# Kernel tuning notes

Hardware: AMD Instinct MI355X
Metric: run time of the kernel (lower is better)

## Reference

```python
import jax, jax.numpy as jnp
import numpy as np

NUM_HEADS = 12
THETA = 10000.0


def _rope(x, pos):
    # x: [B, H, S, dk]; interleaved even/odd pair rotation
    dk = x.shape[-1]
    freqs = THETA ** (-jnp.arange(dk // 2, dtype=jnp.float32) * 2.0 / dk)  # [dk/2]
    ang = pos.astype(jnp.float32)[:, None] * freqs                         # [S, dk/2]
    cos, sin = jnp.cos(ang), jnp.sin(ang)
    x1, x2 = x[..., 0::2], x[..., 1::2]
    rot = jnp.stack([x1 * cos - x2 * sin, x1 * sin + x2 * cos], axis=-1)
    return rot.reshape(x.shape)


def setup_inputs() -> dict:
    key = jax.random.key(0)
    ks = jax.random.split(key, 5)
    B, S, D = 4, 2048, 768
    w_scale = 1.0 / np.sqrt(D).astype(np.float32)
    x = jax.random.normal(ks[0], (B, S, D), dtype=jnp.float32)
    Wq = jax.random.normal(ks[1], (D, D), dtype=jnp.float32) * w_scale
    Wk = jax.random.normal(ks[2], (D, D), dtype=jnp.float32) * w_scale
    Wv = jax.random.normal(ks[3], (D, D), dtype=jnp.float32) * w_scale
    Wo = jax.random.normal(ks[4], (D, D), dtype=jnp.float32) * w_scale
    token_positions = jnp.arange(S, dtype=jnp.int32)
    return {"x": x, "Wq": Wq, "Wk": Wk, "Wv": Wv, "Wo": Wo,
            "token_positions": token_positions}


def reference(x, Wq, Wk, Wv, Wo, token_positions):
    B, S, D = x.shape
    H = NUM_HEADS
    dk = D // H
    # bias-free linear layers: y = x @ W^T (torch Linear weight convention)
    q = (x @ Wq.T).reshape(B, S, H, dk).transpose(0, 2, 1, 3)  # [B,H,S,dk]
    k = (x @ Wk.T).reshape(B, S, H, dk).transpose(0, 2, 1, 3)
    v = (x @ Wv.T).reshape(B, S, H, dk).transpose(0, 2, 1, 3)
    q = _rope(q, token_positions)
    k = _rope(k, token_positions)
    scores = jnp.einsum('bhqd,bhkd->bhqk', q, k) / np.float32(np.sqrt(dk))
    causal = jnp.tril(jnp.ones((S, S), dtype=bool))
    scores = jnp.where(causal, scores, -jnp.inf)
    attn = jax.nn.softmax(scores, axis=-1)                      # [B,H,S,S]
    out = jnp.einsum('bhqk,bhkd->bhqd', attn, v)
    out = out.transpose(0, 2, 1, 3).reshape(B, S, D)
    return out @ Wo.T
```

## Files before the change

### kernel.cpp

```cpp
#include <hip/hip_runtime.h>
#include <cstdint>
#include <cstddef>

#define NTOK 8192
#define SLEN 2048
#define DM   768
#define NH   12
#define DKH  64

typedef __attribute__((ext_vector_type(8))) short bf16x8;
typedef __attribute__((ext_vector_type(4))) float f32x4;

__device__ __forceinline__ float b2f(unsigned short u) {
  return __uint_as_float(((unsigned)u) << 16);
}
__device__ __forceinline__ unsigned short f2b(float f) {
  unsigned u = __float_as_uint(f);
  u += 0x7fffu + ((u >> 16) & 1u);
  return (unsigned short)(u >> 16);
}
__device__ __forceinline__ unsigned cvtpk(float lo, float hi) {
  unsigned r;
  asm("v_cvt_pk_bf16_f32 %0, %1, %2" : "=v"(r) : "v"(lo), "v"(hi));
  return r;
}

__device__ __forceinline__ void gld16(const void* g, void* l) {
  __builtin_amdgcn_global_load_lds(
      (const __attribute__((address_space(1))) void*)g,
      (__attribute__((address_space(3))) void*)l, 16, 0, 0);
}

#define TILE_BAR() do {                                   \
    asm volatile("s_waitcnt vmcnt(0)" ::: "memory");      \
    __builtin_amdgcn_s_barrier();                         \
    __builtin_amdgcn_sched_barrier(0);                    \
  } while (0)

__global__ void cast_bf16_kernel(const float* __restrict__ in,
                                 unsigned short* __restrict__ out, int n8) {
  int i = blockIdx.x * blockDim.x + threadIdx.x;
  if (i >= n8) return;
  const float4* p = (const float4*)(in + (size_t)i * 8);
  float4 a = p[0], b = p[1];
  union { unsigned short h[8]; bf16x8 v; } u;
  u.h[0] = f2b(a.x); u.h[1] = f2b(a.y); u.h[2] = f2b(a.z); u.h[3] = f2b(a.w);
  u.h[4] = f2b(b.x); u.h[5] = f2b(b.y); u.h[6] = f2b(b.z); u.h[7] = f2b(b.w);
  *(bf16x8*)(out + (size_t)i * 8) = u.v;
}

__device__ __forceinline__ void stv(float* p, float v) { *p = v; }
__device__ __forceinline__ void stv(unsigned short* p, float v) { *p = f2b(v); }

template <typename CT>
__global__ __launch_bounds__(256, 2) void gemm_bt_kernel(
    const unsigned short* __restrict__ A,
    const unsigned short* __restrict__ B0, const unsigned short* __restrict__ B1,
    const unsigned short* __restrict__ B2,
    CT* __restrict__ C0, CT* __restrict__ C1, CT* __restrict__ C2,
    int N, int K, const int* __restrict__ pos, int do_rope) {
  const unsigned short* Bp = (blockIdx.z == 0) ? B0 : (blockIdx.z == 1) ? B1 : B2;
  CT* Cp = (blockIdx.z == 0) ? C0 : (blockIdx.z == 1) ? C1 : C2;
  const int tid = threadIdx.x, wid = tid >> 6, lane = tid & 63;
  const int lrow = lane & 15, lk8 = (lane >> 4) << 3;
  const int m0 = blockIdx.y * 128, n0 = blockIdx.x * 128;
  const int wm = (wid >> 1) * 64, wn = (wid & 1) * 64;
  const int sr = lane >> 3, sc = (lane & 7) * 8;
  __shared__ unsigned short At[128 * 64];
  __shared__ unsigned short Bt[128 * 64];
  f32x4 acc[4][4] = {};
  for (int k0 = 0; k0 < K; k0 += 64) {
    __syncthreads();
#pragma unroll
    for (int i = 0; i < 4; ++i) {
      int r = (wid * 4 + i) * 8 + sr;
      int k = sc ^ ((r & 7) << 3);
      gld16(A  + (size_t)(m0 + r) * K + k0 + k, &At[(wid * 4 + i) * 512]);
      gld16(Bp + (size_t)(n0 + r) * K + k0 + k, &Bt[(wid * 4 + i) * 512]);
    }
    __syncthreads();
    bf16x8 af[2][4], bfr[2][4];
#pragma unroll
    for (int ks = 0; ks < 2; ++ks)
#pragma unroll
      for (int mi = 0; mi < 4; ++mi) {
        int ra = wm + mi * 16 + lrow;
        af[ks][mi]  = *(const bf16x8*)&At[ra * 64 + ((ks * 32 + lk8) ^ ((ra & 7) << 3))];
        int rb = wn + mi * 16 + lrow;
        bfr[ks][mi] = *(const bf16x8*)&Bt[rb * 64 + ((ks * 32 + lk8) ^ ((rb & 7) << 3))];
      }
#pragma unroll
    for (int ks = 0; ks < 2; ++ks)
#pragma unroll
      for (int mi = 0; mi < 4; ++mi)
#pragma unroll
        for (int ni = 0; ni < 4; ++ni)
          acc[mi][ni] = __builtin_amdgcn_mfma_f32_16x16x32_bf16(
              af[ks][mi], bfr[ks][ni], acc[mi][ni], 0, 0, 0);
  }

  const bool ropeq = do_rope && (blockIdx.z < 2);
  if (ropeq) {
    float frq[4];
#pragma unroll
    for (int ni = 0; ni < 4; ++ni)
      frq[ni] = exp2f((float)(((n0 + wn + ni * 16 + lrow) & 63) >> 1) *
                      -0.4152410118609203f);
#pragma unroll
    for (int mi = 0; mi < 4; ++mi)
#pragma unroll
      for (int r = 0; r < 4; ++r) {
        int row = m0 + wm + mi * 16 + (lane >> 4) * 4 + r;
        float ps = (float)pos[row & (SLEN - 1)];
#pragma unroll
        for (int ni = 0; ni < 4; ++ni) {
          float v = acc[mi][ni][r];
          float prt = __shfl_xor(v, 1);
          float sn, cs;
          __sincosf(ps * frq[ni], &sn, &cs);
          acc[mi][ni][r] = (lrow & 1) ? fmaf(prt, sn, v * cs)
                                      : fmaf(v, cs, -prt * sn);
        }
      }
  }

#pragma unroll
  for (int mi = 0; mi < 4; ++mi)
#pragma unroll
    for (int ni = 0; ni < 4; ++ni)
#pragma unroll
      for (int r = 0; r < 4; ++r) {
        int row = m0 + wm + mi * 16 + (lane >> 4) * 4 + r;
        int col = n0 + wn + ni * 16 + lrow;
        stv(Cp + (size_t)row * N + col, acc[mi][ni][r]);
      }
}

__global__ void transpose_v_kernel(const unsigned short* __restrict__ V,
                                   unsigned short* __restrict__ VT) {
  const int tt = blockIdx.x, bh = blockIdx.y;
  const int b = bh / NH, h = bh - b * NH;
  const unsigned short* src = V + ((size_t)b * SLEN + tt * 64) * DM + h * DKH;
  unsigned short* dst = VT + (size_t)bh * DKH * SLEN + tt * 64;
  __shared__ unsigned short lds[64][72];
  const int tid = threadIdx.x;
  const int r = tid >> 2, cq = tid & 3;
#pragma unroll
  for (int pass = 0; pass < 2; ++pass) {
    int c = cq * 8 + pass * 32;
    *(bf16x8*)&lds[r][c] = *(const bf16x8*)&src[(size_t)r * DM + c];
  }
  __syncthreads();
  const int d = tid >> 2;
#pragma unroll
  for (int pass = 0; pass < 2; ++pass) {
    int s0 = cq * 8 + pass * 32;
    union { unsigned short h[8]; bf16x8 v; } o;
#pragma unroll
    for (int j = 0; j < 8; ++j) {
      int pi = pass * 32 + 16 * (j >> 2) + 4 * cq + (j & 3);
      o.h[j] = lds[pi][d];
    }
    *(bf16x8*)&dst[(size_t)d * SLEN + s0] = o.v;
  }
}

__global__ __launch_bounds__(256, 2) void attn_kernel(
    const unsigned short* __restrict__ Q, const unsigned short* __restrict__ Kg,
    const unsigned short* __restrict__ VT, unsigned short* __restrict__ O) {
  const int bh = blockIdx.x;
  const int qt = 15 - (int)blockIdx.y;
  const int b = bh / NH, h = bh - b * NH;
  const size_t base = ((size_t)b * SLEN) * DM + h * DKH;
  const size_t vbase = (size_t)bh * DKH * SLEN;
  const int tid = threadIdx.x, wid = tid >> 6, lane = tid & 63;
  const int lrow = lane & 15, g = lane >> 4;

  __shared__ unsigned short Kt[2][64 * 64];
  __shared__ unsigned short Vt[2][64 * 64];

  bf16x8 qf[2][2];
#pragma unroll
  for (int mi = 0; mi < 2; ++mi)
#pragma unroll
    for (int ks = 0; ks < 2; ++ks) {
      const int qrow = qt * 128 + wid * 32 + mi * 16 + lrow;
      union { unsigned short h[8]; bf16x8 v; } u;
      u.v = *(const bf16x8*)&Q[base + (size_t)qrow * DM + ks * 32 + g * 8];
#pragma unroll
      for (int j = 0; j < 8; ++j)
        u.h[j] = f2b(b2f(u.h[j]) * 0.18033688011112042f);
      qf[mi][ks] = u.v;
    }

  f32x4 oacc[2][4] = {};
  float m_run[2] = {-1e30f, -1e30f};
  float l_part[2] = {0.f, 0.f};
  const int qg0 = qt * 128 + wid * 32 + lrow;
  const int nkt = 2 * qt + 2;

  const int srow = wid * 8 + (lane >> 3);
  const int scol = (lane & 7) * 8;

  auto stage = [&](int kt, int buf) {
#pragma unroll
    for (int rnd = 0; rnd < 2; ++rnd) {
      int r = rnd * 32 + srow;
      int c = scol ^ ((r & 7) << 3);
      gld16(Kg + base + (size_t)(kt * 64 + r) * DM + c,
            &Kt[buf][(rnd * 32 + wid * 8) * 64]);
    }
#pragma unroll
    for (int rnd = 0; rnd < 2; ++rnd) {
      int d = rnd * 32 + srow;
      int c = scol ^ ((d & 7) << 3);
      gld16(VT + vbase + (size_t)d * SLEN + kt * 64 + c,
            &Vt[buf][(rnd * 32 + wid * 8) * 64]);
    }
  };

  auto compute = [&](int kt, int buf) {
    const bool active = !(kt == 2 * qt + 1 && wid < 2);
    if (!active) return;
    f32x4 sa[2][4] = {};
    const unsigned short* Ks = Kt[buf];
    __builtin_amdgcn_s_setprio(1);
#pragma unroll
    for (int ks = 0; ks < 2; ++ks)
#pragma unroll
      for (int ni = 0; ni < 4; ++ni) {
        const int krow = ni * 16 + lrow;
        bf16x8 kf = *(const bf16x8*)
            &Ks[krow * 64 + ((ks * 32 + g * 8) ^ ((krow & 7) << 3))];
#pragma unroll
        for (int mi = 0; mi < 2; ++mi)
          sa[mi][ni] = __builtin_amdgcn_mfma_f32_16x16x32_bf16(
              kf, qf[mi][ks], sa[mi][ni], 0, 0, 0);
      }
    __builtin_amdgcn_s_setprio(0);

    const bool need_mask = (kt * 64 + 64 > qt * 128 + wid * 32);
    if (need_mask) {
      const int kb = kt * 64 + g * 4;
#pragma unroll
      for (int mi = 0; mi < 2; ++mi) {
        const int qg = qg0 + mi * 16;
#pragma unroll
        for (int ni = 0; ni < 4; ++ni)
#pragma unroll
          for (int r = 0; r < 4; ++r)
            if (kb + ni * 16 + r > qg) sa[mi][ni][r] = -1e30f;
      }
    }

    float mx[2];
#pragma unroll
    for (int mi = 0; mi < 2; ++mi) {
      f32x4 t01, t23;
#pragma unroll
      for (int r = 0; r < 4; ++r) {
        t01[r] = fmaxf(sa[mi][0][r], sa[mi][1][r]);
        t23[r] = fmaxf(sa[mi][2][r], sa[mi][3][r]);
      }
      float a = fmaxf(fmaxf(t01[0], t23[0]), fmaxf(t01[1], t23[1]));
      float c = fmaxf(fmaxf(t01[2], t23[2]), fmaxf(t01[3], t23[3]));
      mx[mi] = fmaxf(a, c);
    }

    const int viol = (mx[0] > m_run[0] + 8.f) || (mx[1] > m_run[1] + 8.f);
    if (__any(viol)) {
#pragma unroll
      for (int mi = 0; mi < 2; ++mi) {
        float mr = fmaxf(mx[mi], __shfl_xor(mx[mi], 16));
        mr = fmaxf(mr, __shfl_xor(mr, 32));
        float mn = fmaxf(m_run[mi], mr);
        float scl = exp2f(m_run[mi] - mn);
        m_run[mi] = mn;
        l_part[mi] *= scl;
#pragma unroll
        for (int ni = 0; ni < 4; ++ni) oacc[mi][ni] *= scl;
      }
    }

#pragma unroll
    for (int mi = 0; mi < 2; ++mi) {
      float s0 = 0.f;
#pragma unroll
      for (int ni = 0; ni < 4; ++ni)
#pragma unroll
        for (int r = 0; r < 4; ++r) {
          float e = exp2f(sa[mi][ni][r] - m_run[mi]);
          sa[mi][ni][r] = e;
          s0 += e;
        }
      l_part[mi] += s0;
    }

    bf16x8 pf[2][2];
#pragma unroll
    for (int mi = 0; mi < 2; ++mi)
#pragma unroll
      for (int ks = 0; ks < 2; ++ks) {
        union { unsigned u[4]; bf16x8 v; } uu;
        uu.u[0] = cvtpk(sa[mi][2 * ks][0],     sa[mi][2 * ks][1]);
        uu.u[1] = cvtpk(sa[mi][2 * ks][2],     sa[mi][2 * ks][3]);
        uu.u[2] = cvtpk(sa[mi][2 * ks + 1][0], sa[mi][2 * ks + 1][1]);
        uu.u[3] = cvtpk(sa[mi][2 * ks + 1][2], sa[mi][2 * ks + 1][3]);
        pf[mi][ks] = uu.v;
      }

    const unsigned short* Vs = Vt[buf];
    __builtin_amdgcn_s_setprio(1);
#pragma unroll
    for (int ks = 0; ks < 2; ++ks)
#pragma unroll
      for (int ni = 0; ni < 4; ++ni) {
        const int d = ni * 16 + lrow;
        bf16x8 vf = *(const bf16x8*)
            &Vs[d * 64 + ((ks * 32 + g * 8) ^ ((d & 7) << 3))];
#pragma unroll
        for (int mi = 0; mi < 2; ++mi)
          oacc[mi][ni] = __builtin_amdgcn_mfma_f32_16x16x32_bf16(
              vf, pf[mi][ks], oacc[mi][ni], 0, 0, 0);
      }
    __builtin_amdgcn_s_setprio(0);
  };

  stage(0, 0);
  TILE_BAR();
  for (int kt = 0; kt < nkt; ++kt) {
    const int cur = kt & 1;
    if (kt + 1 < nkt) stage(kt + 1, cur ^ 1);
    compute(kt, cur);
    TILE_BAR();
  }

#pragma unroll
  for (int mi = 0; mi < 2; ++mi) {
    float l = l_part[mi];
    l += __shfl_xor(l, 16);
    l += __shfl_xor(l, 32);
    const float inv = 1.f / l;
    const int qrow = qt * 128 + wid * 32 + mi * 16 + lrow;
#pragma unroll
    for (int ni = 0; ni < 4; ++ni) {
      union { unsigned u[2]; ushort4 s; } o;
      o.u[0] = cvtpk(oacc[mi][ni][0] * inv, oacc[mi][ni][1] * inv);
      o.u[1] = cvtpk(oacc[mi][ni][2] * inv, oacc[mi][ni][3] * inv);
      *(ushort4*)&O[base + (size_t)qrow * DM + ni * 16 + g * 4] = o.s;
    }
  }
}

extern "C" void kernel_launch(void* const* d_in, const int* in_sizes, int n_in,
                              void* d_out, int out_size, void* d_ws, size_t ws_size,
                              hipStream_t stream) {
  const float* x  = (const float*)d_in[0];
  const float* Wq = (const float*)d_in[1];
  const float* Wk = (const float*)d_in[2];
  const float* Wv = (const float*)d_in[3];
  const float* Wo = (const float*)d_in[4];
  const int* pos  = (const int*)d_in[5];
  float* out = (float*)d_out;

  char* ws = (char*)d_ws;
  size_t off = 0;
  auto carve = [&](size_t bytes) -> void* {
    void* p = ws + off;
    off += (bytes + 255) & ~(size_t)255;
    return p;
  };
  unsigned short* xb  = (unsigned short*)carve((size_t)NTOK * DM * 2);
  unsigned short* wqb = (unsigned short*)carve((size_t)DM * DM * 2);
  unsigned short* wkb = (unsigned short*)carve((size_t)DM * DM * 2);
  unsigned short* wvb = (unsigned short*)carve((size_t)DM * DM * 2);
  unsigned short* wob = (unsigned short*)carve((size_t)DM * DM * 2);
  unsigned short* Qb  = (unsigned short*)carve((size_t)NTOK * DM * 2);
  unsigned short* Kb  = (unsigned short*)carve((size_t)NTOK * DM * 2);
  unsigned short* Vb  = (unsigned short*)carve((size_t)NTOK * DM * 2);
  unsigned short* Ab  = (unsigned short*)carve((size_t)NTOK * DM * 2);
  unsigned short* VTb = (unsigned short*)carve((size_t)4 * NH * DKH * SLEN * 2);

  const int n8x = NTOK * DM / 8;
  const int n8w = DM * DM / 8;
  cast_bf16_kernel<<<dim3((n8x + 255) / 256), dim3(256), 0, stream>>>(x, xb, n8x);
  cast_bf16_kernel<<<dim3((n8w + 255) / 256), dim3(256), 0, stream>>>(Wq, wqb, n8w);
  cast_bf16_kernel<<<dim3((n8w + 255) / 256), dim3(256), 0, stream>>>(Wk, wkb, n8w);
  cast_bf16_kernel<<<dim3((n8w + 255) / 256), dim3(256), 0, stream>>>(Wv, wvb, n8w);
  cast_bf16_kernel<<<dim3((n8w + 255) / 256), dim3(256), 0, stream>>>(Wo, wob, n8w);

  gemm_bt_kernel<unsigned short><<<dim3(6, 64, 3), dim3(256), 0, stream>>>(
      xb, wqb, wkb, wvb, Qb, Kb, Vb, DM, DM, pos, 1);

  transpose_v_kernel<<<dim3(SLEN / 64, 4 * NH), dim3(256), 0, stream>>>(Vb, VTb);

  attn_kernel<<<dim3(48, 16), dim3(256), 0, stream>>>(Qb, Kb, VTb, Ab);

  gemm_bt_kernel<float><<<dim3(6, 64, 1), dim3(256), 0, stream>>>(
      Ab, wob, wob, wob, out, out, out, DM, DM, pos, 0);
}
```

Measured before the change: 141.4 us.

## Double-buffer GEMM tiles, triple-buffer attention K/V, merge weight casts

The GEMM now double-buffers its A/B LDS tiles and prefetches the next k-tile while computing the current one, replacing the two syncthreads per iteration. The attention kernel moves to a three-deep K/V ring with a partial vmcnt wait, so one barrier per tile overlaps loads with compute. The four weight-cast launches are merged into one launch. In exchange, LDS use per block roughly doubles in the GEMM and grows by half in attention, which could lower occupancy. The cast merge also relies on the four weight buffers being laid out contiguously by the carve allocator.

Measured after the change: 146.3 us. +3.5%, slower.

```diff
diff --git a/kernel.cpp b/kernel.cpp
--- a/kernel.cpp
+++ b/kernel.cpp
@@ -31,8 +31,13 @@
       (__attribute__((address_space(3))) void*)l, 16, 0, 0);
 }
 
-#define TILE_BAR() do {                                   \
+#define BAR_DRAIN() do {                                  \
     asm volatile("s_waitcnt vmcnt(0)" ::: "memory");      \
+    __builtin_amdgcn_s_barrier();                         \
+    __builtin_amdgcn_sched_barrier(0);                    \
+  } while (0)
+#define BAR_KEEP4() do {                                  \
+    asm volatile("s_waitcnt vmcnt(4)" ::: "memory");      \
     __builtin_amdgcn_s_barrier();                         \
     __builtin_amdgcn_sched_barrier(0);                    \
   } while (0)
@@ -47,6 +52,24 @@
   u.h[0] = f2b(a.x); u.h[1] = f2b(a.y); u.h[2] = f2b(a.z); u.h[3] = f2b(a.w);
   u.h[4] = f2b(b.x); u.h[5] = f2b(b.y); u.h[6] = f2b(b.z); u.h[7] = f2b(b.w);
   *(bf16x8*)(out + (size_t)i * 8) = u.v;
+}
+
+__global__ void cast4_bf16_kernel(const float* __restrict__ s0,
+                                  const float* __restrict__ s1,
+                                  const float* __restrict__ s2,
+                                  const float* __restrict__ s3,
+                                  unsigned short* __restrict__ out, int n8) {
+  int i = blockIdx.x * blockDim.x + threadIdx.x;
+  if (i >= n8) return;
+  const float* src = (blockIdx.y == 0) ? s0 : (blockIdx.y == 1) ? s1
+                    : (blockIdx.y == 2) ? s2 : s3;
+  unsigned short* o = out + (size_t)blockIdx.y * DM * DM + (size_t)i * 8;
+  const float4* p = (const float4*)(src + (size_t)i * 8);
+  float4 a = p[0], b = p[1];
+  union { unsigned short h[8]; bf16x8 v; } u;
+  u.h[0] = f2b(a.x); u.h[1] = f2b(a.y); u.h[2] = f2b(a.z); u.h[3] = f2b(a.w);
+  u.h[4] = f2b(b.x); u.h[5] = f2b(b.y); u.h[6] = f2b(b.z); u.h[7] = f2b(b.w);
+  *(bf16x8*)o = u.v;
 }
 
 __device__ __forceinline__ void stv(float* p, float v) { *p = v; }
@@ -66,28 +89,36 @@
   const int m0 = blockIdx.y * 128, n0 = blockIdx.x * 128;
   const int wm = (wid >> 1) * 64, wn = (wid & 1) * 64;
   const int sr = lane >> 3, sc = (lane & 7) * 8;
-  __shared__ unsigned short At[128 * 64];
-  __shared__ unsigned short Bt[128 * 64];
+  __shared__ unsigned short At[2][128 * 64];
+  __shared__ unsigned short Bt[2][128 * 64];
   f32x4 acc[4][4] = {};
-  for (int k0 = 0; k0 < K; k0 += 64) {
-    __syncthreads();
+
+  auto stage = [&](int kk, int buf) {
+    const int k0 = kk * 64;
 #pragma unroll
     for (int i = 0; i < 4; ++i) {
       int r = (wid * 4 + i) * 8 + sr;
       int k = sc ^ ((r & 7) << 3);
-      gld16(A  + (size_t)(m0 + r) * K + k0 + k, &At[(wid * 4 + i) * 512]);
-      gld16(Bp + (size_t)(n0 + r) * K + k0 + k, &Bt[(wid * 4 + i) * 512]);
-    }
-    __syncthreads();
+      gld16(A  + (size_t)(m0 + r) * K + k0 + k, &At[buf][(wid * 4 + i) * 512]);
+      gld16(Bp + (size_t)(n0 + r) * K + k0 + k, &Bt[buf][(wid * 4 + i) * 512]);
+    }
+  };
+
+  const int nk = K / 64;
+  stage(0, 0);
+  BAR_DRAIN();
+  for (int kk = 0; kk < nk; ++kk) {
+    const int cur = kk & 1;
+    if (kk + 1 < nk) stage(kk + 1, cur ^ 1);
     bf16x8 af[2][4], bfr[2][4];
 #pragma unroll
     for (int ks = 0; ks < 2; ++ks)
 #pragma unroll
       for (int mi = 0; mi < 4; ++mi) {
         int ra = wm + mi * 16 + lrow;
-        af[ks][mi]  = *(const bf16x8*)&At[ra * 64 + ((ks * 32 + lk8) ^ ((ra & 7) << 3))];
+        af[ks][mi]  = *(const bf16x8*)&At[cur][ra * 64 + ((ks * 32 + lk8) ^ ((ra & 7) << 3))];
         int rb = wn + mi * 16 + lrow;
-        bfr[ks][mi] = *(const bf16x8*)&Bt[rb * 64 + ((ks * 32 + lk8) ^ ((rb & 7) << 3))];
+        bfr[ks][mi] = *(const bf16x8*)&Bt[cur][rb * 64 + ((ks * 32 + lk8) ^ ((rb & 7) << 3))];
       }
 #pragma unroll
     for (int ks = 0; ks < 2; ++ks)
@@ -97,6 +128,7 @@
         for (int ni = 0; ni < 4; ++ni)
           acc[mi][ni] = __builtin_amdgcn_mfma_f32_16x16x32_bf16(
               af[ks][mi], bfr[ks][ni], acc[mi][ni], 0, 0, 0);
+    BAR_DRAIN();
   }
 
   const bool ropeq = do_rope && (blockIdx.z < 2);
@@ -176,8 +208,8 @@
   const int tid = threadIdx.x, wid = tid >> 6, lane = tid & 63;
   const int lrow = lane & 15, g = lane >> 4;
 
-  __shared__ unsigned short Kt[2][64 * 64];
-  __shared__ unsigned short Vt[2][64 * 64];
+  __shared__ unsigned short Kt[3][64 * 64];
+  __shared__ unsigned short Vt[3][64 * 64];
 
   bf16x8 qf[2][2];
 #pragma unroll
@@ -327,12 +359,14 @@
   };
 
   stage(0, 0);
-  TILE_BAR();
   for (int kt = 0; kt < nkt; ++kt) {
-    const int cur = kt & 1;
-    if (kt + 1 < nkt) stage(kt + 1, cur ^ 1);
-    compute(kt, cur);
-    TILE_BAR();
+    if (kt + 1 < nkt) {
+      stage(kt + 1, (kt + 1) % 3);
+      BAR_KEEP4();
+    } else {
+      BAR_DRAIN();
+    }
+    compute(kt, kt % 3);
   }
 
 #pragma unroll
@@ -384,10 +418,8 @@
   const int n8x = NTOK * DM / 8;
   const int n8w = DM * DM / 8;
   cast_bf16_kernel<<<dim3((n8x + 255) / 256), dim3(256), 0, stream>>>(x, xb, n8x);
-  cast_bf16_kernel<<<dim3((n8w + 255) / 256), dim3(256), 0, stream>>>(Wq, wqb, n8w);
-  cast_bf16_kernel<<<dim3((n8w + 255) / 256), dim3(256), 0, stream>>>(Wk, wkb, n8w);
-  cast_bf16_kernel<<<dim3((n8w + 255) / 256), dim3(256), 0, stream>>>(Wv, wvb, n8w);
-  cast_bf16_kernel<<<dim3((n8w + 255) / 256), dim3(256), 0, stream>>>(Wo, wob, n8w);
+  cast4_bf16_kernel<<<dim3((n8w + 255) / 256, 4), dim3(256), 0, stream>>>(
+      Wq, Wk, Wv, Wo, wqb, n8w);
 
   gemm_bt_kernel<unsigned short><<<dim3(6, 64, 3), dim3(256), 0, stream>>>(
       xb, wqb, wkb, wvb, Qb, Kb, Vb, DM, DM, pos, 1);
```

## Shrink attention Q tile to 64 rows, balance causal order, fuse weight casts

Applied to the files above, without the earlier changes.

The attention kernel now gives each block 64 query rows instead of 128, so each wave owns 16 rows. This doubles the grid to 48x32, and launch bounds are raised to allow three blocks per CU. Tiles are interleaved so long and short causal tiles alternate, and the inactive-wave special case goes away. Four weight-cast launches are merged into one kernel with a y-dimension selector. The smaller tiles cut per-block work imbalance and raise occupancy, but each K/V tile is now staged twice as often per query row, which adds LDS and global traffic.

Result: slower. 147.7 us (+4.5%).

```diff
diff --git a/kernel.cpp b/kernel.cpp
--- a/kernel.cpp
+++ b/kernel.cpp
@@ -31,7 +31,7 @@
       (__attribute__((address_space(3))) void*)l, 16, 0, 0);
 }
 
-#define TILE_BAR() do {                                   \
+#define BAR_DRAIN() do {                                  \
     asm volatile("s_waitcnt vmcnt(0)" ::: "memory");      \
     __builtin_amdgcn_s_barrier();                         \
     __builtin_amdgcn_sched_barrier(0);                    \
@@ -47,6 +47,24 @@
   u.h[0] = f2b(a.x); u.h[1] = f2b(a.y); u.h[2] = f2b(a.z); u.h[3] = f2b(a.w);
   u.h[4] = f2b(b.x); u.h[5] = f2b(b.y); u.h[6] = f2b(b.z); u.h[7] = f2b(b.w);
   *(bf16x8*)(out + (size_t)i * 8) = u.v;
+}
+
+__global__ void cast4_bf16_kernel(const float* __restrict__ s0,
+                                  const float* __restrict__ s1,
+                                  const float* __restrict__ s2,
+                                  const float* __restrict__ s3,
+                                  unsigned short* __restrict__ out, int n8) {
+  int i = blockIdx.x * blockDim.x + threadIdx.x;
+  if (i >= n8) return;
+  const float* src = (blockIdx.y == 0) ? s0 : (blockIdx.y == 1) ? s1
+                    : (blockIdx.y == 2) ? s2 : s3;
+  unsigned short* o = out + (size_t)blockIdx.y * DM * DM + (size_t)i * 8;
+  const float4* p = (const float4*)(src + (size_t)i * 8);
+  float4 a = p[0], b = p[1];
+  union { unsigned short h[8]; bf16x8 v; } u;
+  u.h[0] = f2b(a.x); u.h[1] = f2b(a.y); u.h[2] = f2b(a.z); u.h[3] = f2b(a.w);
+  u.h[4] = f2b(b.x); u.h[5] = f2b(b.y); u.h[6] = f2b(b.z); u.h[7] = f2b(b.w);
+  *(bf16x8*)o = u.v;
 }
 
 __device__ __forceinline__ void stv(float* p, float v) { *p = v; }
@@ -165,11 +183,12 @@
   }
 }
 
-__global__ __launch_bounds__(256, 2) void attn_kernel(
+__global__ __launch_bounds__(256, 3) void attn_kernel(
     const unsigned short* __restrict__ Q, const unsigned short* __restrict__ Kg,
     const unsigned short* __restrict__ VT, unsigned short* __restrict__ O) {
   const int bh = blockIdx.x;
-  const int qt = 15 - (int)blockIdx.y;
+  const int y = blockIdx.y;
+  const int qt = (y & 1) ? (y >> 1) : (31 - (y >> 1));
   const int b = bh / NH, h = bh - b * NH;
   const size_t base = ((size_t)b * SLEN) * DM + h * DKH;
   const size_t vbase = (size_t)bh * DKH * SLEN;
@@ -179,25 +198,22 @@
   __shared__ unsigned short Kt[2][64 * 64];
   __shared__ unsigned short Vt[2][64 * 64];
 
-  bf16x8 qf[2][2];
-#pragma unroll
-  for (int mi = 0; mi < 2; ++mi)
-#pragma unroll
-    for (int ks = 0; ks < 2; ++ks) {
-      const int qrow = qt * 128 + wid * 32 + mi * 16 + lrow;
-      union { unsigned short h[8]; bf16x8 v; } u;
-      u.v = *(const bf16x8*)&Q[base + (size_t)qrow * DM + ks * 32 + g * 8];
-#pragma unroll
-      for (int j = 0; j < 8; ++j)
-        u.h[j] = f2b(b2f(u.h[j]) * 0.18033688011112042f);
-      qf[mi][ks] = u.v;
-    }
-
-  f32x4 oacc[2][4] = {};
-  float m_run[2] = {-1e30f, -1e30f};
-  float l_part[2] = {0.f, 0.f};
-  const int qg0 = qt * 128 + wid * 32 + lrow;
-  const int nkt = 2 * qt + 2;
+  bf16x8 qf[2];
+#pragma unroll
+  for (int ks = 0; ks < 2; ++ks) {
+    const int qrow = qt * 64 + wid * 16 + lrow;
+    union { unsigned short h[8]; bf16x8 v; } u;
+    u.v = *(const bf16x8*)&Q[base + (size_t)qrow * DM + ks * 32 + g * 8];
+#pragma unroll
+    for (int j = 0; j < 8; ++j)
+      u.h[j] = f2b(b2f(u.h[j]) * 0.18033688011112042f);
+    qf[ks] = u.v;
+  }
+
+  f32x4 oacc[4] = {};
+  float m_run = -1e30f, l_part = 0.f;
+  const int qg = qt * 64 + wid * 16 + lrow;
+  const int nkt = qt + 1;
 
   const int srow = wid * 8 + (lane >> 3);
   const int scol = (lane & 7) * 8;
@@ -220,9 +236,7 @@
   };
 
   auto compute = [&](int kt, int buf) {
-    const bool active = !(kt == 2 * qt + 1 && wid < 2);
-    if (!active) return;
-    f32x4 sa[2][4] = {};
+    f32x4 sa[4] = {};
     const unsigned short* Ks = Kt[buf];
     __builtin_amdgcn_s_setprio(1);
 #pragma unroll
@@ -232,82 +246,61 @@
         const int krow = ni * 16 + lrow;
         bf16x8 kf = *(const bf16x8*)
             &Ks[krow * 64 + ((ks * 32 + g * 8) ^ ((krow & 7) << 3))];
-#pragma unroll
-        for (int mi = 0; mi < 2; ++mi)
-          sa[mi][ni] = __builtin_amdgcn_mfma_f32_16x16x32_bf16(
-              kf, qf[mi][ks], sa[mi][ni], 0, 0, 0);
+        sa[ni] = __builtin_amdgcn_mfma_f32_16x16x32_bf16(
+            kf, qf[ks], sa[ni], 0, 0, 0);
       }
     __builtin_amdgcn_s_setprio(0);
 
-    const bool need_mask = (kt * 64 + 64 > qt * 128 + wid * 32);
-    if (need_mask) {
+    if (kt == qt) {
       const int kb = kt * 64 + g * 4;
 #pragma unroll
-      for (int mi = 0; mi < 2; ++mi) {
-        const int qg = qg0 + mi * 16;
-#pragma unroll
-        for (int ni = 0; ni < 4; ++ni)
-#pragma unroll
-          for (int r = 0; r < 4; ++r)
-            if (kb + ni * 16 + r > qg) sa[mi][ni][r] = -1e30f;
-      }
-    }
-
-    float mx[2];
-#pragma unroll
-    for (int mi = 0; mi < 2; ++mi) {
-      f32x4 t01, t23;
+      for (int ni = 0; ni < 4; ++ni)
+#pragma unroll
+        for (int r = 0; r < 4; ++r)
+          if (kb + ni * 16 + r > qg) sa[ni][r] = -1e30f;
+    }
+
+    f32x4 t01, t23;
+#pragma unroll
+    for (int r = 0; r < 4; ++r) {
+      t01[r] = fmaxf(sa[0][r], sa[1][r]);
+      t23[r] = fmaxf(sa[2][r], sa[3][r]);
+    }
+    float mx = fmaxf(fmaxf(fmaxf(t01[0], t23[0]), fmaxf(t01[1], t23[1])),
+                     fmaxf(fmaxf(t01[2], t23[2]), fmaxf(t01[3], t23[3])));
+
+    if (__any(mx > m_run + 8.f)) {
+      float mr = fmaxf(mx, __shfl_xor(mx, 16));
+      mr = fmaxf(mr, __shfl_xor(mr, 32));
+      float mn = fmaxf(m_run, mr);
+      float scl = exp2f(m_run - mn);
+      m_run = mn;
+      l_part *= scl;
+#pragma unroll
+      for (int ni = 0; ni < 4; ++ni) oacc[ni] *= scl;
+    }
+
+    float s0 = 0.f;
+#pragma unroll
+    for (int ni = 0; ni < 4; ++ni)
 #pragma unroll
       for (int r = 0; r < 4; ++r) {
-        t01[r] = fmaxf(sa[mi][0][r], sa[mi][1][r]);
-        t23[r] = fmaxf(sa[mi][2][r], sa[mi][3][r]);
-      }
-      float a = fmaxf(fmaxf(t01[0], t23[0]), fmaxf(t01[1], t23[1]));
-      float c = fmaxf(fmaxf(t01[2], t23[2]), fmaxf(t01[3], t23[3]));
-      mx[mi] = fmaxf(a, c);
-    }
-
-    const int viol = (mx[0] > m_run[0] + 8.f) || (mx[1] > m_run[1] + 8.f);
-    if (__any(viol)) {
-#pragma unroll
-      for (int mi = 0; mi < 2; ++mi) {
-        float mr = fmaxf(mx[mi], __shfl_xor(mx[mi], 16));
-        mr = fmaxf(mr, __shfl_xor(mr, 32));
-        float mn = fmaxf(m_run[mi], mr);
-        float scl = exp2f(m_run[mi] - mn);
-        m_run[mi] = mn;
-        l_part[mi] *= scl;
-#pragma unroll
-        for (int ni = 0; ni < 4; ++ni) oacc[mi][ni] *= scl;
-      }
-    }
-
-#pragma unroll
-    for (int mi = 0; mi < 2; ++mi) {
-      float s0 = 0.f;
-#pragma unroll
-      for (int ni = 0; ni < 4; ++ni)
-#pragma unroll
-        for (int r = 0; r < 4; ++r) {
-          float e = exp2f(sa[mi][ni][r] - m_run[mi]);
-          sa[mi][ni][r] = e;
-          s0 += e;
-        }
-      l_part[mi] += s0;
-    }
-
-    bf16x8 pf[2][2];
-#pragma unroll
-    for (int mi = 0; mi < 2; ++mi)
-#pragma unroll
-      for (int ks = 0; ks < 2; ++ks) {
-        union { unsigned u[4]; bf16x8 v; } uu;
-        uu.u[0] = cvtpk(sa[mi][2 * ks][0],     sa[mi][2 * ks][1]);
-        uu.u[1] = cvtpk(sa[mi][2 * ks][2],     sa[mi][2 * ks][3]);
-        uu.u[2] = cvtpk(sa[mi][2 * ks + 1][0], sa[mi][2 * ks + 1][1]);
-        uu.u[3] = cvtpk(sa[mi][2 * ks + 1][2], sa[mi][2 * ks + 1][3]);
-        pf[mi][ks] = uu.v;
-      }
+        float e = exp2f(sa[ni][r] - m_run);
+        sa[ni][r] = e;
+        s0 += e;
+      }
+    l_part += s0;
+
+    bf16x8 pf[2];
+#pragma unroll
+    for (int ks = 0; ks < 2; ++ks) {
+      union { unsigned u[4]; bf16x8 v; } uu;
+      uu.u[0] = cvtpk(sa[2 * ks][0],     sa[2 * ks][1]);
+      uu.u[1] = cvtpk(sa[2 * ks][2],     sa[2 * ks][3]);
+      uu.u[2] = cvtpk(sa[2 * ks + 1][0], sa[2 * ks + 1][1]);
+      uu.u[3] = cvtpk(sa[2 * ks + 1][2], sa[2 * ks + 1][3]);
+      pf[ks] = uu.v;
+    }
 
     const unsigned short* Vs = Vt[buf];
     __builtin_amdgcn_s_setprio(1);
@@ -318,37 +311,32 @@
         const int d = ni * 16 + lrow;
         bf16x8 vf = *(const bf16x8*)
             &Vs[d * 64 + ((ks * 32 + g * 8) ^ ((d & 7) << 3))];
-#pragma unroll
-        for (int mi = 0; mi < 2; ++mi)
-          oacc[mi][ni] = __builtin_amdgcn_mfma_f32_16x16x32_bf16(
-              vf, pf[mi][ks], oacc[mi][ni], 0, 0, 0);
+        oacc[ni] = __builtin_amdgcn_mfma_f32_16x16x32_bf16(
+            vf, pf[ks], oacc[ni], 0, 0, 0);
       }
     __builtin_amdgcn_s_setprio(0);
   };
 
   stage(0, 0);
-  TILE_BAR();
+  BAR_DRAIN();
   for (int kt = 0; kt < nkt; ++kt) {
     const int cur = kt & 1;
     if (kt + 1 < nkt) stage(kt + 1, cur ^ 1);
     compute(kt, cur);
-    TILE_BAR();
-  }
-
-#pragma unroll
-  for (int mi = 0; mi < 2; ++mi) {
-    float l = l_part[mi];
-    l += __shfl_xor(l, 16);
-    l += __shfl_xor(l, 32);
-    const float inv = 1.f / l;
-    const int qrow = qt * 128 + wid * 32 + mi * 16 + lrow;
-#pragma unroll
-    for (int ni = 0; ni < 4; ++ni) {
-      union { unsigned u[2]; ushort4 s; } o;
-      o.u[0] = cvtpk(oacc[mi][ni][0] * inv, oacc[mi][ni][1] * inv);
-      o.u[1] = cvtpk(oacc[mi][ni][2] * inv, oacc[mi][ni][3] * inv);
-      *(ushort4*)&O[base + (size_t)qrow * DM + ni * 16 + g * 4] = o.s;
-    }
+    BAR_DRAIN();
+  }
+
+  float l = l_part;
+  l += __shfl_xor(l, 16);
+  l += __shfl_xor(l, 32);
+  const float inv = 1.f / l;
+  const int qrow = qt * 64 + wid * 16 + lrow;
+#pragma unroll
+  for (int ni = 0; ni < 4; ++ni) {
+    union { unsigned u[2]; ushort4 s; } o;
+    o.u[0] = cvtpk(oacc[ni][0] * inv, oacc[ni][1] * inv);
+    o.u[1] = cvtpk(oacc[ni][2] * inv, oacc[ni][3] * inv);
+    *(ushort4*)&O[base + (size_t)qrow * DM + ni * 16 + g * 4] = o.s;
   }
 }
 
@@ -384,17 +372,15 @@
   const int n8x = NTOK * DM / 8;
   const int n8w = DM * DM / 8;
   cast_bf16_kernel<<<dim3((n8x + 255) / 256), dim3(256), 0, stream>>>(x, xb, n8x);
-  cast_bf16_kernel<<<dim3((n8w + 255) / 256), dim3(256), 0, stream>>>(Wq, wqb, n8w);
-  cast_bf16_kernel<<<dim3((n8w + 255) / 256), dim3(256), 0, stream>>>(Wk, wkb, n8w);
-  cast_bf16_kernel<<<dim3((n8w + 255) / 256), dim3(256), 0, stream>>>(Wv, wvb, n8w);
-  cast_bf16_kernel<<<dim3((n8w + 255) / 256), dim3(256), 0, stream>>>(Wo, wob, n8w);
+  cast4_bf16_kernel<<<dim3((n8w + 255) / 256, 4), dim3(256), 0, stream>>>(
+      Wq, Wk, Wv, Wo, wqb, n8w);
 
   gemm_bt_kernel<unsigned short><<<dim3(6, 64, 3), dim3(256), 0, stream>>>(
       xb, wqb, wkb, wvb, Qb, Kb, Vb, DM, DM, pos, 1);
 
   transpose_v_kernel<<<dim3(SLEN / 64, 4 * NH), dim3(256), 0, stream>>>(Vb, VTb);
 
-  attn_kernel<<<dim3(48, 16), dim3(256), 0, stream>>>(Qb, Kb, VTb, Ab);
+  attn_kernel<<<dim3(48, 32), dim3(256), 0, stream>>>(Qb, Kb, VTb, Ab);
 
   gemm_bt_kernel<float><<<dim3(6, 64, 1), dim3(256), 0, stream>>>(
       Ab, wob, wob, wob, out, out, out, DM, DM, pos, 0);
```
